# Kernel tuning notes

Hardware: AMD Instinct MI355X
Metric: run time of the kernel (lower is better)

## Reference

```python
import jax, jax.numpy as jnp
import numpy as np

B, N, D = 4, 4096, 768
SCALE = 1.0 / np.sqrt(D).astype(np.float32)


def setup_inputs() -> dict:
    key = jax.random.key(0)
    k1, k2, k3 = jax.random.split(key, 3)
    x = jax.random.normal(k1, (B, N, D), dtype=jnp.float32)
    w_qkv = jax.random.normal(k2, (D, 3 * D), dtype=jnp.float32) * (1.0 / np.sqrt(D))
    b_qkv = jnp.zeros((3 * D,), dtype=jnp.float32)
    w_out = jax.random.normal(k3, (D, D), dtype=jnp.float32) * (1.0 / np.sqrt(D))
    b_out = jnp.zeros((D,), dtype=jnp.float32)
    return {"x": x, "w_qkv": w_qkv, "b_qkv": b_qkv, "w_out": w_out, "b_out": b_out}


def reference(x, w_qkv, b_qkv, w_out, b_out):
    # fused QKV projection: [B,N,3D]
    qkv = jnp.einsum("bnd,de->bne", x, w_qkv) + b_qkv
    q, k, v = jnp.split(qkv, 3, axis=-1)          # each [B,N,D]
    # scaled dot-product attention (single head)
    scores = jnp.einsum("bnd,bmd->bnm", q, k) * SCALE  # [B,N,N]
    attn = jax.nn.softmax(scores, axis=-1)
    ctx = jnp.einsum("bnm,bmd->bnd", attn, v)          # [B,N,D]
    out = jnp.einsum("bnd,de->bne", ctx, w_out) + b_out
    return out
```

## Files before the change

### kernel.cpp

```cpp
#include <hip/hip_runtime.h>
#include <cstdint>
#include <cstddef>

#define BB 4
#define NN 4096
#define DD 768
#define EE 2304
#define MTOT 16384
static constexpr float ATT_SCALE = 0.03608439182435161f;

typedef _Float16 v8h __attribute__((ext_vector_type(8)));
typedef _Float16 v4h __attribute__((ext_vector_type(4)));
typedef float v4f __attribute__((ext_vector_type(4)));
typedef uint32_t v4u __attribute__((ext_vector_type(4)));

#define LGKM0 asm volatile("s_waitcnt lgkmcnt(0)" ::: "memory")
#define SCHED0 __builtin_amdgcn_sched_barrier(0)
#define BAR __builtin_amdgcn_s_barrier()

enum { EPI_QKV = 0, EPI_F16 = 1, EPI_OUT = 2, EPI_PV = 3 };

template <int EPI, int SWZ = 0>
__global__ __launch_bounds__(512, 2) void gemm256(
    const _Float16* __restrict__ A, int lda, size_t zA,
    const _Float16* __restrict__ Bt, int ldb, size_t zB,
    int K,
    float* __restrict__ c_f32,
    _Float16* __restrict__ c_f16,
    int ldc, size_t zC, size_t chalf,
    const float* __restrict__ bias,
    _Float16* __restrict__ q_out,
    _Float16* __restrict__ k_out,
    _Float16* __restrict__ v_out) {
  __shared__ __align__(16) _Float16 As[2][256 * 64];
  __shared__ __align__(16) _Float16 Bs[2][256 * 64];

  const int tid = threadIdx.x;
  const int wid = tid >> 6, lane = tid & 63;
  const int wr = wid >> 2, wc = wid & 3;
  const int lq = lane >> 4, lr = lane & 15;

  int bx = blockIdx.x, by = blockIdx.y;
  if constexpr (SWZ == 1) {
    const int lin = bx + (by << 4);
    const int xcd = lin & 7, j = lin >> 3;
    bx = (xcd & 1) * 8 + (j & 7);
    by = (xcd >> 1) * 4 + (j >> 3);
  }
  const int m0 = bx * 256, n0 = by * 256;
  const int z = blockIdx.z;
  int bidx, koff;
  if constexpr (EPI == EPI_PV) {
    bidx = z & 1;
    koff = (z >> 1) * K;
  } else {
    bidx = z;
    koff = 0;
  }

  const _Float16* Ab = A + (size_t)bidx * zA + (size_t)m0 * lda + koff;
  const _Float16* Bb = Bt + (size_t)bidx * zB + (size_t)n0 * ldb + koff;

  int gA[4], gB[4], lds_off[4];
#pragma unroll
  for (int i = 0; i < 4; ++i) {
    const int c = i * 512 + tid;
    const int r = c >> 3, kc = c & 7;
    gA[i] = r * lda + kc * 8;
    gB[i] = r * ldb + kc * 8;
    lds_off[i] = r * 64 + ((kc ^ (r & 7)) << 3);
  }

  int aoff[8], boff[4];
#pragma unroll
  for (int t = 0; t < 8; ++t) {
    const int ra = wr * 128 + t * 16 + lr;
    aoff[t] = ra * 64 + ((lq ^ (ra & 7)) << 3);
  }
#pragma unroll
  for (int n = 0; n < 4; ++n) {
    const int rb = wc * 64 + n * 16 + lr;
    boff[n] = rb * 64 + ((lq ^ (rb & 7)) << 3);
  }

  v4f acc[8][4] = {};
  const int NT = K / 64;

  v4u va[4], vb[4];

  auto loadT = [&](int kt) {
    const _Float16* a = Ab + kt * 64;
    const _Float16* b = Bb + kt * 64;
#pragma unroll
    for (int i = 0; i < 4; ++i) {
      va[i] = *(const v4u*)(a + gA[i]);
      vb[i] = *(const v4u*)(b + gB[i]);
    }
  };
  auto writeT = [&](int slot) {
#pragma unroll
    for (int i = 0; i < 4; ++i) {
      *(v4u*)(&As[slot][0] + lds_off[i]) = va[i];
      *(v4u*)(&Bs[slot][0] + lds_off[i]) = vb[i];
    }
  };
  auto mfma16 = [&](const v8h* af_, const v8h* bf_, int mbase) {
#pragma unroll
    for (int mt = 0; mt < 4; ++mt)
#pragma unroll
      for (int nt = 0; nt < 4; ++nt)
        acc[mbase + mt][nt] = __builtin_amdgcn_mfma_f32_16x16x32_f16(
            af_[mt], bf_[nt], acc[mbase + mt][nt], 0, 0, 0);
  };

  loadT(0);
  writeT(0);
  loadT(1);
  LGKM0;
  SCHED0;
  BAR;
  SCHED0;

  for (int t = 0; t < NT; ++t) {
    const int cur = t & 1, ns = cur ^ 1;
    const _Float16* Ac = &As[cur][0];
    const _Float16* Bc = &Bs[cur][0];
    v8h a_[4], b0_[4], b1_[4];

#pragma unroll
    for (int i = 0; i < 4; ++i) a_[i] = *(const v8h*)(Ac + aoff[i]);
#pragma unroll
    for (int i = 0; i < 4; ++i) b0_[i] = *(const v8h*)(Bc + boff[i]);
    __builtin_amdgcn_s_setprio(1);
    mfma16(a_, b0_, 0);
    __builtin_amdgcn_s_setprio(0);

#pragma unroll
    for (int i = 0; i < 4; ++i) a_[i] = *(const v8h*)(Ac + aoff[4 + i]);
    __builtin_amdgcn_s_setprio(1);
    mfma16(a_, b0_, 4);
    __builtin_amdgcn_s_setprio(0);

#pragma unroll
    for (int i = 0; i < 4; ++i) a_[i] = *(const v8h*)(Ac + (aoff[i] ^ 32));
#pragma unroll
    for (int i = 0; i < 4; ++i) b1_[i] = *(const v8h*)(Bc + (boff[i] ^ 32));
    __builtin_amdgcn_s_setprio(1);
    mfma16(a_, b1_, 0);
    __builtin_amdgcn_s_setprio(0);

#pragma unroll
    for (int i = 0; i < 4; ++i) a_[i] = *(const v8h*)(Ac + (aoff[4 + i] ^ 32));
    __builtin_amdgcn_s_setprio(1);
    mfma16(a_, b1_, 4);
    __builtin_amdgcn_s_setprio(0);

    if (t + 1 < NT) {
      writeT(ns);
      if (t + 2 < NT) loadT(t + 2);
    }
    LGKM0;
    SCHED0;
    BAR;
    SCHED0;
  }

  float* cf = nullptr;
  _Float16* ch = nullptr;
  if constexpr (EPI == EPI_PV)
    cf = c_f32 + (size_t)(z >> 1) * chalf + (size_t)bidx * zC;
  else if constexpr (EPI == EPI_OUT)
    cf = c_f32 + (size_t)bidx * zC;
  else if constexpr (EPI == EPI_F16)
    ch = c_f16 + (size_t)bidx * zC;

#pragma unroll
  for (int mt = 0; mt < 8; ++mt) {
#pragma unroll
    for (int nt = 0; nt < 4; ++nt) {
#pragma unroll
      for (int rg = 0; rg < 4; ++rg) {
        const int gm = m0 + wr * 128 + mt * 16 + lq * 4 + rg;
        const int gn = n0 + wc * 64 + nt * 16 + lr;
        float v = acc[mt][nt][rg];
        if constexpr (EPI == EPI_QKV) {
          v += bias[gn];
          if (gn < DD) {
            q_out[(size_t)gm * DD + gn] = (_Float16)(v * ATT_SCALE);
          } else if (gn < 2 * DD) {
            k_out[(size_t)gm * DD + (gn - DD)] = (_Float16)v;
          } else {
            v_out[(size_t)gm * DD + (gn - 2 * DD)] = (_Float16)v;
          }
        } else if constexpr (EPI == EPI_F16) {
          ch[(size_t)gm * ldc + gn] = (_Float16)v;
        } else {
          cf[(size_t)gm * ldc + gn] = (EPI == EPI_OUT) ? v + bias[gn] : v;
        }
      }
    }
  }
}

__global__ __launch_bounds__(256) void reduce_ctx(const float* __restrict__ h0,
                                                  const float* __restrict__ h1,
                                                  _Float16* __restrict__ out,
                                                  int n4) {
  int i = blockIdx.x * blockDim.x + threadIdx.x;
  if (i < n4) {
    v4f a = ((const v4f*)h0)[i];
    v4f b = ((const v4f*)h1)[i];
    v4h o;
#pragma unroll
    for (int j = 0; j < 4; ++j) o[j] = (_Float16)(a[j] + b[j]);
    ((v4h*)out)[i] = o;
  }
}

__global__ __launch_bounds__(256) void softmax_rows_f16(_Float16* __restrict__ S) {
  _Float16* row = S + (size_t)blockIdx.y * NN * NN + (size_t)blockIdx.x * NN;
  const int tid = threadIdx.x;
  const int lane = tid & 63, wid = tid >> 6;

  float f[16];
  float m = -3.0e38f;
#pragma unroll
  for (int i = 0; i < 2; ++i) {
    v8h v = ((const v8h*)row)[tid + i * 256];
#pragma unroll
    for (int j = 0; j < 8; ++j) {
      f[i * 8 + j] = (float)v[j];
      m = fmaxf(m, f[i * 8 + j]);
    }
  }
#pragma unroll
  for (int off = 32; off > 0; off >>= 1) m = fmaxf(m, __shfl_xor(m, off));
  __shared__ float redm[4], reds[4];
  if (lane == 0) redm[wid] = m;
  __syncthreads();
  m = fmaxf(fmaxf(redm[0], redm[1]), fmaxf(redm[2], redm[3]));

  float sum = 0.f;
#pragma unroll
  for (int i = 0; i < 16; ++i) {
    f[i] = __expf(f[i] - m);
    sum += f[i];
  }
#pragma unroll
  for (int off = 32; off > 0; off >>= 1) sum += __shfl_xor(sum, off);
  if (lane == 0) reds[wid] = sum;
  __syncthreads();
  sum = reds[0] + reds[1] + reds[2] + reds[3];
  const float inv = 1.0f / sum;
#pragma unroll
  for (int i = 0; i < 2; ++i) {
    v8h o;
#pragma unroll
    for (int j = 0; j < 8; ++j) o[j] = (_Float16)(f[i * 8 + j] * inv);
    ((v8h*)row)[tid + i * 256] = o;
  }
}

__global__ __launch_bounds__(256) void cvt_f16(const float* __restrict__ in,
                                               _Float16* __restrict__ out, int n4) {
  int i = blockIdx.x * blockDim.x + threadIdx.x;
  if (i < n4) {
    v4f v = ((const v4f*)in)[i];
    v4h o;
#pragma unroll
    for (int j = 0; j < 4; ++j) o[j] = (_Float16)v[j];
    ((v4h*)out)[i] = o;
  }
}

__global__ __launch_bounds__(256) void transpose_cvt(const float* __restrict__ in,
                                                     _Float16* __restrict__ out,
                                                     int R, int C) {
  __shared__ float tile[32][33];
  const int bx = blockIdx.x * 32;
  const int by = blockIdx.y * 32;
  const int tx = threadIdx.x & 31, ty = threadIdx.x >> 5;
#pragma unroll
  for (int i = 0; i < 32; i += 8)
    tile[ty + i][tx] = in[(size_t)(by + ty + i) * C + (bx + tx)];
  __syncthreads();
#pragma unroll
  for (int i = 0; i < 32; i += 8)
    out[(size_t)(bx + ty + i) * R + (by + tx)] = (_Float16)tile[tx][ty + i];
}

__global__ __launch_bounds__(256) void transpose_v(const _Float16* __restrict__ in,
                                                   _Float16* __restrict__ out) {
  __shared__ _Float16 tile[32][33];
  const int b = blockIdx.z;
  const _Float16* src = in + (size_t)b * NN * DD;
  _Float16* dst = out + (size_t)b * NN * DD;
  const int bx = blockIdx.x * 32;
  const int by = blockIdx.y * 32;
  const int tx = threadIdx.x & 31, ty = threadIdx.x >> 5;
#pragma unroll
  for (int i = 0; i < 32; i += 8)
    tile[ty + i][tx] = src[(size_t)(by + ty + i) * DD + (bx + tx)];
  __syncthreads();
#pragma unroll
  for (int i = 0; i < 32; i += 8)
    dst[(size_t)(bx + ty + i) * NN + (by + tx)] = tile[tx][ty + i];
}

extern "C" void kernel_launch(void* const* d_in, const int* in_sizes, int n_in,
                              void* d_out, int out_size, void* d_ws, size_t ws_size,
                              hipStream_t stream) {
  const float* x = (const float*)d_in[0];
  const float* w_qkv = (const float*)d_in[1];
  const float* b_qkv = (const float*)d_in[2];
  const float* w_out = (const float*)d_in[3];
  const float* b_out = (const float*)d_in[4];
  float* out = (float*)d_out;
  char* ws = (char*)d_ws;

  _Float16* xh    = (_Float16*)(ws + 0);
  _Float16* wqkvh = (_Float16*)(ws + 25165824);
  _Float16* wouth = (_Float16*)(ws + 28704768);
  _Float16* Qh    = (_Float16*)(ws + 29884416);
  _Float16* Kh    = (_Float16*)(ws + 55050240);
  _Float16* Vh    = (_Float16*)(ws + 80216064);
  _Float16* Sh    = (_Float16*)(ws + 105381888);
  _Float16* Vth   = (_Float16*)(ws + 0);
  _Float16* Ch    = (_Float16*)(ws + 80216064);

  const size_t zQK = (size_t)NN * DD;
  const size_t zS = (size_t)NN * NN;
  const size_t zCtx = (size_t)NN * DD;
  const size_t chalf = 2 * zCtx;

  cvt_f16<<<dim3((MTOT * DD / 4) / 256), 256, 0, stream>>>(x, xh, MTOT * DD / 4);
  transpose_cvt<<<dim3(EE / 32, DD / 32), 256, 0, stream>>>(w_qkv, wqkvh, DD, EE);
  transpose_cvt<<<dim3(DD / 32, DD / 32), 256, 0, stream>>>(w_out, wouth, DD, DD);

  gemm256<EPI_QKV><<<dim3(MTOT / 256, EE / 256), 512, 0, stream>>>(
      xh, DD, 0, wqkvh, DD, 0, DD, nullptr, nullptr, 0, 0, 0, b_qkv, Qh, Kh, Vh);

  transpose_v<<<dim3(DD / 32, NN / 32, BB), 256, 0, stream>>>(Vh, Vth);

  for (int c = 0; c < BB / 2; ++c) {
    const _Float16* Qc = Qh + (size_t)c * 2 * zQK;
    const _Float16* Kc = Kh + (size_t)c * 2 * zQK;
    const _Float16* Vtc = Vth + (size_t)c * 2 * zQK;
    gemm256<EPI_F16, 1><<<dim3(NN / 256, NN / 256, 2), 512, 0, stream>>>(
        Qc, DD, zQK, Kc, DD, zQK, DD, nullptr, Sh, NN, zS, 0, nullptr, nullptr,
        nullptr, nullptr);
    softmax_rows_f16<<<dim3(NN, 2), 256, 0, stream>>>(Sh);
    gemm256<EPI_PV><<<dim3(NN / 256, DD / 256, 4), 512, 0, stream>>>(
        Sh, NN, zS, Vtc, NN, zQK, NN / 2, out, nullptr, DD, zCtx, chalf,
        nullptr, nullptr, nullptr, nullptr);
    reduce_ctx<<<dim3((int)(chalf / 4 / 256)), 256, 0, stream>>>(
        out, out + chalf, Ch + (size_t)c * 2 * zQK, (int)(chalf / 4));
  }

  gemm256<EPI_OUT><<<dim3(MTOT / 256, DD / 256), 512, 0, stream>>>(
      Ch, DD, 0, wouth, DD, 0, DD, out, nullptr, DD, 0, 0, b_out, nullptr,
      nullptr, nullptr);
}
```

Before: 546.4 us.

## Fuse softmax into QK^T epilogue stats and PV operand load

Removes the standalone row-softmax pass over the fp16 score matrix. The QK^T GEMM epilogue now computes per-tile row max and sum-of-exp and writes them to a partial-stats buffer. A small combine kernel merges the 16 column-tile partials into a final max and reciprocal sum per row. The PV GEMM applies exp(s - m) * inv to the raw scores while staging them into LDS. This saves one full read and write of the large score matrix. In exchange it adds exp work inside the PV GEMM's LDS-write path and a reduction in the QK^T epilogue, and it reuses workspace for the stats.

```diff
diff --git a/kernel.cpp b/kernel.cpp
--- a/kernel.cpp
+++ b/kernel.cpp
@@ -18,7 +18,7 @@
 #define SCHED0 __builtin_amdgcn_sched_barrier(0)
 #define BAR __builtin_amdgcn_s_barrier()
 
-enum { EPI_QKV = 0, EPI_F16 = 1, EPI_OUT = 2, EPI_PV = 3 };
+enum { EPI_QKV = 0, EPI_QKT = 1, EPI_OUT = 2, EPI_PV = 3 };
 
 template <int EPI, int SWZ = 0>
 __global__ __launch_bounds__(512, 2) void gemm256(
@@ -31,7 +31,9 @@
     const float* __restrict__ bias,
     _Float16* __restrict__ q_out,
     _Float16* __restrict__ k_out,
-    _Float16* __restrict__ v_out) {
+    _Float16* __restrict__ v_out,
+    float* __restrict__ sp,
+    const float* __restrict__ sf) {
   __shared__ __align__(16) _Float16 As[2][256 * 64];
   __shared__ __align__(16) _Float16 Bs[2][256 * 64];
 
@@ -71,6 +73,17 @@
     lds_off[i] = r * 64 + ((kc ^ (r & 7)) << 3);
   }
 
+  float stm[4] = {}, sti[4] = {};
+  if constexpr (EPI == EPI_PV) {
+#pragma unroll
+    for (int i = 0; i < 4; ++i) {
+      const int r = (i * 512 + tid) >> 3;
+      const float* p = sf + ((size_t)bidx * NN + m0 + r) * 2;
+      stm[i] = p[0];
+      sti[i] = p[1];
+    }
+  }
+
   int aoff[8], boff[4];
 #pragma unroll
   for (int t = 0; t < 8; ++t) {
@@ -100,7 +113,16 @@
   auto writeT = [&](int slot) {
 #pragma unroll
     for (int i = 0; i < 4; ++i) {
-      *(v4u*)(&As[slot][0] + lds_off[i]) = va[i];
+      if constexpr (EPI == EPI_PV) {
+        v8h h = *reinterpret_cast<v8h*>(&va[i]);
+        v8h o;
+#pragma unroll
+        for (int j = 0; j < 8; ++j)
+          o[j] = (_Float16)(__expf((float)h[j] - stm[i]) * sti[i]);
+        *(v8h*)(&As[slot][0] + lds_off[i]) = o;
+      } else {
+        *(v4u*)(&As[slot][0] + lds_off[i]) = va[i];
+      }
       *(v4u*)(&Bs[slot][0] + lds_off[i]) = vb[i];
     }
   };
@@ -165,13 +187,53 @@
     SCHED0;
   }
 
+  if constexpr (EPI == EPI_QKT) {
+    float* sred = (float*)&As[0][0];
+#pragma unroll
+    for (int mt = 0; mt < 8; ++mt) {
+#pragma unroll
+      for (int rg = 0; rg < 4; ++rg) {
+        float mx = fmaxf(fmaxf(acc[mt][0][rg], acc[mt][1][rg]),
+                         fmaxf(acc[mt][2][rg], acc[mt][3][rg]));
+#pragma unroll
+        for (int off = 1; off < 16; off <<= 1) mx = fmaxf(mx, __shfl_xor(mx, off));
+        float s = 0.f;
+#pragma unroll
+        for (int nt = 0; nt < 4; ++nt) s += __expf(acc[mt][nt][rg] - mx);
+#pragma unroll
+        for (int off = 1; off < 16; off <<= 1) s += __shfl_xor(s, off);
+        if (lr == 0) {
+          const int r = wr * 128 + mt * 16 + lq * 4 + rg;
+          sred[(r * 4 + wc) * 2] = mx;
+          sred[(r * 4 + wc) * 2 + 1] = s;
+        }
+      }
+    }
+    __syncthreads();
+    if (tid < 256) {
+      float m = -3.0e38f, l = 0.f;
+      float pm[4], pl[4];
+#pragma unroll
+      for (int w = 0; w < 4; ++w) {
+        pm[w] = sred[(tid * 4 + w) * 2];
+        pl[w] = sred[(tid * 4 + w) * 2 + 1];
+        m = fmaxf(m, pm[w]);
+      }
+#pragma unroll
+      for (int w = 0; w < 4; ++w) l += pl[w] * __expf(pm[w] - m);
+      const size_t o = (((size_t)bidx * 16 + by) * NN + (m0 + tid)) * 2;
+      sp[o] = m;
+      sp[o + 1] = l;
+    }
+  }
+
   float* cf = nullptr;
   _Float16* ch = nullptr;
   if constexpr (EPI == EPI_PV)
     cf = c_f32 + (size_t)(z >> 1) * chalf + (size_t)bidx * zC;
   else if constexpr (EPI == EPI_OUT)
     cf = c_f32 + (size_t)bidx * zC;
-  else if constexpr (EPI == EPI_F16)
+  else if constexpr (EPI == EPI_QKT)
     ch = c_f16 + (size_t)bidx * zC;
 
 #pragma unroll
@@ -192,7 +254,7 @@
           } else {
             v_out[(size_t)gm * DD + (gn - 2 * DD)] = (_Float16)v;
           }
-        } else if constexpr (EPI == EPI_F16) {
+        } else if constexpr (EPI == EPI_QKT) {
           ch[(size_t)gm * ldc + gn] = (_Float16)v;
         } else {
           cf[(size_t)gm * ldc + gn] = (EPI == EPI_OUT) ? v + bias[gn] : v;
@@ -200,6 +262,27 @@
       }
     }
   }
+}
+
+__global__ __launch_bounds__(256) void combine_stats(const float* __restrict__ sp,
+                                                     float* __restrict__ sf) {
+  const int row = blockIdx.x * 256 + threadIdx.x;
+  const int b = row >> 12;
+  const int r = row & (NN - 1);
+  float mv[16], lv[16];
+  float m = -3.0e38f;
+#pragma unroll
+  for (int k = 0; k < 16; ++k) {
+    const size_t idx = (((size_t)b * 16 + k) * NN + r) * 2;
+    mv[k] = sp[idx];
+    lv[k] = sp[idx + 1];
+    m = fmaxf(m, mv[k]);
+  }
+  float l = 0.f;
+#pragma unroll
+  for (int k = 0; k < 16; ++k) l += lv[k] * __expf(mv[k] - m);
+  sf[(size_t)row * 2] = m;
+  sf[(size_t)row * 2 + 1] = 1.0f / l;
 }
 
 __global__ __launch_bounds__(256) void reduce_ctx(const float* __restrict__ h0,
@@ -214,50 +297,6 @@
 #pragma unroll
     for (int j = 0; j < 4; ++j) o[j] = (_Float16)(a[j] + b[j]);
     ((v4h*)out)[i] = o;
-  }
-}
-
-__global__ __launch_bounds__(256) void softmax_rows_f16(_Float16* __restrict__ S) {
-  _Float16* row = S + (size_t)blockIdx.y * NN * NN + (size_t)blockIdx.x * NN;
-  const int tid = threadIdx.x;
-  const int lane = tid & 63, wid = tid >> 6;
-
-  float f[16];
-  float m = -3.0e38f;
-#pragma unroll
-  for (int i = 0; i < 2; ++i) {
-    v8h v = ((const v8h*)row)[tid + i * 256];
-#pragma unroll
-    for (int j = 0; j < 8; ++j) {
-      f[i * 8 + j] = (float)v[j];
-      m = fmaxf(m, f[i * 8 + j]);
-    }
-  }
-#pragma unroll
-  for (int off = 32; off > 0; off >>= 1) m = fmaxf(m, __shfl_xor(m, off));
-  __shared__ float redm[4], reds[4];
-  if (lane == 0) redm[wid] = m;
-  __syncthreads();
-  m = fmaxf(fmaxf(redm[0], redm[1]), fmaxf(redm[2], redm[3]));
-
-  float sum = 0.f;
-#pragma unroll
-  for (int i = 0; i < 16; ++i) {
-    f[i] = __expf(f[i] - m);
-    sum += f[i];
-  }
-#pragma unroll
-  for (int off = 32; off > 0; off >>= 1) sum += __shfl_xor(sum, off);
-  if (lane == 0) reds[wid] = sum;
-  __syncthreads();
-  sum = reds[0] + reds[1] + reds[2] + reds[3];
-  const float inv = 1.0f / sum;
-#pragma unroll
-  for (int i = 0; i < 2; ++i) {
-    v8h o;
-#pragma unroll
-    for (int j = 0; j < 8; ++j) o[j] = (_Float16)(f[i * 8 + j] * inv);
-    ((v8h*)row)[tid + i * 256] = o;
   }
 }
 
@@ -327,6 +366,8 @@
   _Float16* Sh    = (_Float16*)(ws + 105381888);
   _Float16* Vth   = (_Float16*)(ws + 0);
   _Float16* Ch    = (_Float16*)(ws + 80216064);
+  float* stats_p  = (float*)(ws + 25165824);
+  float* stats_f  = (float*)(ws + 25165824 + 1048576);
 
   const size_t zQK = (size_t)NN * DD;
   const size_t zS = (size_t)NN * NN;
@@ -338,7 +379,8 @@
   transpose_cvt<<<dim3(DD / 32, DD / 32), 256, 0, stream>>>(w_out, wouth, DD, DD);
 
   gemm256<EPI_QKV><<<dim3(MTOT / 256, EE / 256), 512, 0, stream>>>(
-      xh, DD, 0, wqkvh, DD, 0, DD, nullptr, nullptr, 0, 0, 0, b_qkv, Qh, Kh, Vh);
+      xh, DD, 0, wqkvh, DD, 0, DD, nullptr, nullptr, 0, 0, 0, b_qkv, Qh, Kh, Vh,
+      nullptr, nullptr);
 
   transpose_v<<<dim3(DD / 32, NN / 32, BB), 256, 0, stream>>>(Vh, Vth);
 
@@ -346,18 +388,18 @@
     const _Float16* Qc = Qh + (size_t)c * 2 * zQK;
     const _Float16* Kc = Kh + (size_t)c * 2 * zQK;
     const _Float16* Vtc = Vth + (size_t)c * 2 * zQK;
-    gemm256<EPI_F16, 1><<<dim3(NN / 256, NN / 256, 2), 512, 0, stream>>>(
+    gemm256<EPI_QKT, 1><<<dim3(NN / 256, NN / 256, 2), 512, 0, stream>>>(
         Qc, DD, zQK, Kc, DD, zQK, DD, nullptr, Sh, NN, zS, 0, nullptr, nullptr,
-        nullptr, nullptr);
-    softmax_rows_f16<<<dim3(NN, 2), 256, 0, stream>>>(Sh);
+        nullptr, nullptr, stats_p, nullptr);
+    combine_stats<<<dim3(2 * NN / 256), 256, 0, stream>>>(stats_p, stats_f);
     gemm256<EPI_PV><<<dim3(NN / 256, DD / 256, 4), 512, 0, stream>>>(
         Sh, NN, zS, Vtc, NN, zQK, NN / 2, out, nullptr, DD, zCtx, chalf,
-        nullptr, nullptr, nullptr, nullptr);
+        nullptr, nullptr, nullptr, nullptr, nullptr, stats_f);
     reduce_ctx<<<dim3((int)(chalf / 4 / 256)), 256, 0, stream>>>(
         out, out + chalf, Ch + (size_t)c * 2 * zQK, (int)(chalf / 4));
   }
 
   gemm256<EPI_OUT><<<dim3(MTOT / 256, DD / 256), 512, 0, stream>>>(
       Ch, DD, 0, wouth, DD, 0, DD, out, nullptr, DD, 0, 0, b_out, nullptr,
-      nullptr, nullptr);
-}
+      nullptr, nullptr, nullptr, nullptr);
+}
```

Result: slower. 587.1 us (+7.4%).

## Stage GEMM epilogues through LDS for coalesced stores and fuse V transpose

Applied to the files above, without the earlier changes.

All GEMM epilogues now write accumulators into a swizzled shared-memory tile and then emit wide 16-byte coalesced global stores, replacing scattered per-element stores. The QKV GEMM writes its V tile transposed straight into the layout the PV GEMM needs, so the separate transpose_v kernel and its extra pass over V are removed. Shared memory is unified into one buffer that is reused for the epilogue. The cost is extra barriers and an LDS round trip in the epilogue, plus a workspace layout change that aliases Vth with Ch.

```diff
diff --git a/kernel.cpp b/kernel.cpp
--- a/kernel.cpp
+++ b/kernel.cpp
@@ -18,7 +18,7 @@
 #define SCHED0 __builtin_amdgcn_sched_barrier(0)
 #define BAR __builtin_amdgcn_s_barrier()
 
-enum { EPI_QKV = 0, EPI_F16 = 1, EPI_OUT = 2, EPI_PV = 3 };
+enum { EPI_QKV = 0, EPI_QKT = 1, EPI_OUT = 2, EPI_PV = 3 };
 
 template <int EPI, int SWZ = 0>
 __global__ __launch_bounds__(512, 2) void gemm256(
@@ -32,8 +32,7 @@
     _Float16* __restrict__ q_out,
     _Float16* __restrict__ k_out,
     _Float16* __restrict__ v_out) {
-  __shared__ __align__(16) _Float16 As[2][256 * 64];
-  __shared__ __align__(16) _Float16 Bs[2][256 * 64];
+  __shared__ __align__(16) _Float16 SMEM[65536];
 
   const int tid = threadIdx.x;
   const int wid = tid >> 6, lane = tid & 63;
@@ -98,10 +97,12 @@
     }
   };
   auto writeT = [&](int slot) {
+    _Float16* As = SMEM + slot * 16384;
+    _Float16* Bs = SMEM + 32768 + slot * 16384;
 #pragma unroll
     for (int i = 0; i < 4; ++i) {
-      *(v4u*)(&As[slot][0] + lds_off[i]) = va[i];
-      *(v4u*)(&Bs[slot][0] + lds_off[i]) = vb[i];
+      *(v4u*)(As + lds_off[i]) = va[i];
+      *(v4u*)(Bs + lds_off[i]) = vb[i];
     }
   };
   auto mfma16 = [&](const v8h* af_, const v8h* bf_, int mbase) {
@@ -123,8 +124,8 @@
 
   for (int t = 0; t < NT; ++t) {
     const int cur = t & 1, ns = cur ^ 1;
-    const _Float16* Ac = &As[cur][0];
-    const _Float16* Bc = &Bs[cur][0];
+    const _Float16* Ac = SMEM + cur * 16384;
+    const _Float16* Bc = SMEM + 32768 + cur * 16384;
     v8h a_[4], b0_[4], b1_[4];
 
 #pragma unroll
@@ -165,38 +166,84 @@
     SCHED0;
   }
 
-  float* cf = nullptr;
-  _Float16* ch = nullptr;
-  if constexpr (EPI == EPI_PV)
-    cf = c_f32 + (size_t)(z >> 1) * chalf + (size_t)bidx * zC;
-  else if constexpr (EPI == EPI_OUT)
-    cf = c_f32 + (size_t)bidx * zC;
-  else if constexpr (EPI == EPI_F16)
-    ch = c_f16 + (size_t)bidx * zC;
-
-#pragma unroll
-  for (int mt = 0; mt < 8; ++mt) {
-#pragma unroll
-    for (int nt = 0; nt < 4; ++nt) {
-#pragma unroll
-      for (int rg = 0; rg < 4; ++rg) {
-        const int gm = m0 + wr * 128 + mt * 16 + lq * 4 + rg;
-        const int gn = n0 + wc * 64 + nt * 16 + lr;
-        float v = acc[mt][nt][rg];
-        if constexpr (EPI == EPI_QKV) {
-          v += bias[gn];
-          if (gn < DD) {
-            q_out[(size_t)gm * DD + gn] = (_Float16)(v * ATT_SCALE);
-          } else if (gn < 2 * DD) {
-            k_out[(size_t)gm * DD + (gn - DD)] = (_Float16)v;
-          } else {
-            v_out[(size_t)gm * DD + (gn - 2 * DD)] = (_Float16)v;
+
+  if constexpr (EPI == EPI_QKV || EPI == EPI_QKT) {
+    bool vreg = false;
+    float scl = 1.0f;
+    if constexpr (EPI == EPI_QKV) {
+      vreg = (by >= 6);
+      if (by < 3) scl = ATT_SCALE;
+    }
+#pragma unroll
+    for (int mt = 0; mt < 8; ++mt) {
+#pragma unroll
+      for (int nt = 0; nt < 4; ++nt) {
+#pragma unroll
+        for (int rg = 0; rg < 4; ++rg) {
+          const int rr = wr * 128 + mt * 16 + lq * 4 + rg;
+          const int cc = wc * 64 + nt * 16 + lr;
+          float v = acc[mt][nt][rg];
+          if constexpr (EPI == EPI_QKV) v = (v + bias[n0 + cc]) * scl;
+          const int row = vreg ? cc : rr;
+          const int col = vreg ? rr : cc;
+          SMEM[row * 256 + (col ^ ((row & 7) << 3))] = (_Float16)v;
+        }
+      }
+    }
+    __syncthreads();
+    const int bat = m0 >> 12, mloc = m0 & (NN - 1);
+#pragma unroll
+    for (int i2 = 0; i2 < 16; ++i2) {
+      const int c = i2 * 512 + tid;
+      const int row = c >> 5, cic = c & 31;
+      v8h val = *(const v8h*)(SMEM + row * 256 + ((cic ^ (row & 7)) << 3));
+      if constexpr (EPI == EPI_QKV) {
+        if (by < 3) {
+          *(v8h*)(q_out + (size_t)(m0 + row) * DD + (n0 + cic * 8)) = val;
+        } else if (by < 6) {
+          *(v8h*)(k_out + (size_t)(m0 + row) * DD + (n0 - DD + cic * 8)) = val;
+        } else {
+          *(v8h*)(v_out + (size_t)bat * NN * DD +
+                  (size_t)(n0 - 2 * DD + row) * NN + (mloc + cic * 8)) = val;
+        }
+      } else {
+        _Float16* ch = c_f16 + (size_t)bidx * zC;
+        *(v8h*)(ch + (size_t)(m0 + row) * ldc + (n0 + cic * 8)) = val;
+      }
+    }
+  } else {
+    float* S4 = (float*)SMEM;
+    float* cf;
+    if constexpr (EPI == EPI_PV)
+      cf = c_f32 + (size_t)(z >> 1) * chalf + (size_t)bidx * zC;
+    else
+      cf = c_f32 + (size_t)bidx * zC;
+#pragma unroll
+    for (int h = 0; h < 2; ++h) {
+      if (h) __syncthreads();
+      if (wr == h) {
+#pragma unroll
+        for (int mt = 0; mt < 8; ++mt) {
+#pragma unroll
+          for (int nt = 0; nt < 4; ++nt) {
+#pragma unroll
+            for (int rg = 0; rg < 4; ++rg) {
+              const int row = mt * 16 + lq * 4 + rg;
+              const int cc = wc * 64 + nt * 16 + lr;
+              float v = acc[mt][nt][rg];
+              if constexpr (EPI == EPI_OUT) v += bias[n0 + cc];
+              S4[row * 256 + (cc ^ ((row & 7) << 2))] = v;
+            }
           }
-        } else if constexpr (EPI == EPI_F16) {
-          ch[(size_t)gm * ldc + gn] = (_Float16)v;
-        } else {
-          cf[(size_t)gm * ldc + gn] = (EPI == EPI_OUT) ? v + bias[gn] : v;
         }
+      }
+      __syncthreads();
+#pragma unroll
+      for (int i2 = 0; i2 < 16; ++i2) {
+        const int c = i2 * 512 + tid;
+        const int row = c >> 6, cic = c & 63;
+        v4f val = *(const v4f*)(S4 + row * 256 + ((cic ^ (row & 7)) << 2));
+        *(v4f*)(cf + (size_t)(m0 + h * 128 + row) * ldc + (n0 + cic * 4)) = val;
       }
     }
   }
@@ -287,24 +334,6 @@
 #pragma unroll
   for (int i = 0; i < 32; i += 8)
     out[(size_t)(bx + ty + i) * R + (by + tx)] = (_Float16)tile[tx][ty + i];
-}
-
-__global__ __launch_bounds__(256) void transpose_v(const _Float16* __restrict__ in,
-                                                   _Float16* __restrict__ out) {
-  __shared__ _Float16 tile[32][33];
-  const int b = blockIdx.z;
-  const _Float16* src = in + (size_t)b * NN * DD;
-  _Float16* dst = out + (size_t)b * NN * DD;
-  const int bx = blockIdx.x * 32;
-  const int by = blockIdx.y * 32;
-  const int tx = threadIdx.x & 31, ty = threadIdx.x >> 5;
-#pragma unroll
-  for (int i = 0; i < 32; i += 8)
-    tile[ty + i][tx] = src[(size_t)(by + ty + i) * DD + (bx + tx)];
-  __syncthreads();
-#pragma unroll
-  for (int i = 0; i < 32; i += 8)
-    dst[(size_t)(bx + ty + i) * NN + (by + tx)] = tile[tx][ty + i];
 }
 
 extern "C" void kernel_launch(void* const* d_in, const int* in_sizes, int n_in,
@@ -323,9 +352,8 @@
   _Float16* wouth = (_Float16*)(ws + 28704768);
   _Float16* Qh    = (_Float16*)(ws + 29884416);
   _Float16* Kh    = (_Float16*)(ws + 55050240);
-  _Float16* Vh    = (_Float16*)(ws + 80216064);
+  _Float16* Vth   = (_Float16*)(ws + 80216064);
   _Float16* Sh    = (_Float16*)(ws + 105381888);
-  _Float16* Vth   = (_Float16*)(ws + 0);
   _Float16* Ch    = (_Float16*)(ws + 80216064);
 
   const size_t zQK = (size_t)NN * DD;
@@ -338,15 +366,14 @@
   transpose_cvt<<<dim3(DD / 32, DD / 32), 256, 0, stream>>>(w_out, wouth, DD, DD);
 
   gemm256<EPI_QKV><<<dim3(MTOT / 256, EE / 256), 512, 0, stream>>>(
-      xh, DD, 0, wqkvh, DD, 0, DD, nullptr, nullptr, 0, 0, 0, b_qkv, Qh, Kh, Vh);
-
-  transpose_v<<<dim3(DD / 32, NN / 32, BB), 256, 0, stream>>>(Vh, Vth);
+      xh, DD, 0, wqkvh, DD, 0, DD, nullptr, nullptr, 0, 0, 0, b_qkv, Qh, Kh,
+      Vth);
 
   for (int c = 0; c < BB / 2; ++c) {
     const _Float16* Qc = Qh + (size_t)c * 2 * zQK;
     const _Float16* Kc = Kh + (size_t)c * 2 * zQK;
     const _Float16* Vtc = Vth + (size_t)c * 2 * zQK;
-    gemm256<EPI_F16, 1><<<dim3(NN / 256, NN / 256, 2), 512, 0, stream>>>(
+    gemm256<EPI_QKT, 1><<<dim3(NN / 256, NN / 256, 2), 512, 0, stream>>>(
         Qc, DD, zQK, Kc, DD, zQK, DD, nullptr, Sh, NN, zS, 0, nullptr, nullptr,
         nullptr, nullptr);
     softmax_rows_f16<<<dim3(NN, 2), 256, 0, stream>>>(Sh);
```

Result: no change. 550.1 us (+0.7%).
